# Performance work log

Hardware: AMD Instinct MI355X
Metric: run time of the kernel (lower is better)

The kernel has to match this reference:

```python
import jax, jax.numpy as jnp
import numpy as np

OBS, ACT, H, O, B = 256, 64, 1024, 8, 4096
ALPHA, GAMMA, ACT_LIMIT = 0.2, 0.99, 1.0
LOG_STD_MIN, LOG_STD_MAX = -20.0, 2.0
D = OBS + ACT + O  # intra-Q input dim


def setup_inputs() -> dict:
    key = jax.random.key(0)
    ks = iter(jax.random.split(key, 64))
    w = lambda shape: (jax.random.normal(next(ks), shape) * 0.05).astype(jnp.float32)
    inp = {}
    inp["state"] = jax.random.normal(next(ks), (B, OBS), jnp.float32)
    inp["action"] = jnp.tanh(jax.random.normal(next(ks), (B, ACT), jnp.float32))
    inp["next_state"] = jax.random.normal(next(ks), (B, OBS), jnp.float32)
    inp["reward"] = jax.random.normal(next(ks), (B, 1), jnp.float32)
    inp["done"] = jnp.zeros((B, 1), jnp.float32)
    inp["noise"] = jax.random.normal(next(ks), (B, ACT), jnp.float32)
    inp["option"] = jax.random.randint(next(ks), (B,), 0, O, jnp.int32)
    # online inter-Q (q1,q2 stacked on leading axis): obs -> H -> H -> O
    inp["interq_W1"], inp["interq_b1"] = w((2, OBS, H)), w((2, H))
    inp["interq_W2"], inp["interq_b2"] = w((2, H, H)), w((2, H))
    inp["interq_W3"], inp["interq_b3"] = w((2, H, O)), w((2, O))
    # target inter-Q
    inp["tinterq_W1"], inp["tinterq_b1"] = w((2, OBS, H)), w((2, H))
    inp["tinterq_W2"], inp["tinterq_b2"] = w((2, H, H)), w((2, H))
    inp["tinterq_W3"], inp["tinterq_b3"] = w((2, H, O)), w((2, O))
    # intra-Q (q1,q2 stacked): [obs,act,onehot] -> H -> H -> 1
    inp["intraq_W1"], inp["intraq_b1"] = w((2, D, H)), w((2, H))
    inp["intraq_W2"], inp["intraq_b2"] = w((2, H, H)), w((2, H))
    inp["intraq_W3"], inp["intraq_b3"] = w((2, H, 1)), w((2, 1))
    # per-option squashed-Gaussian policies: obs -> H -> H -> (mu, log_std)
    inp["pol_W1"], inp["pol_b1"] = w((O, OBS, H)), w((O, H))
    inp["pol_W2"], inp["pol_b2"] = w((O, H, H)), w((O, H))
    inp["pol_Wmu"], inp["pol_bmu"] = w((O, H, ACT)), w((O, ACT))
    inp["pol_Wls"], inp["pol_bls"] = w((O, H, ACT)), w((O, ACT))
    # per-option termination (beta) nets: obs -> H -> 1, sigmoid
    inp["beta_W1"], inp["beta_b1"] = w((O, OBS, H)), w((O, H))
    inp["beta_W2"], inp["beta_b2"] = w((O, H, 1)), w((O, 1))
    return inp


def _mlp2_k(x, W1, b1, W2, b2, W3, b3):
    # x: [B,in], params stacked over leading k -> [k,B,out]
    h = jax.nn.relu(jnp.einsum('bi,kih->kbh', x, W1) + b1[:, None, :])
    h = jax.nn.relu(jnp.einsum('kbh,khg->kbg', h, W2) + b2[:, None, :])
    return jnp.einsum('kbg,kgo->kbo', h, W3) + b3[:, None, :]


def _forward(state, action, next_state, reward, done, noise,
             interq_W1, interq_b1, interq_W2, interq_b2, interq_W3, interq_b3,
             tinterq_W1, tinterq_b1, tinterq_W2, tinterq_b2, tinterq_W3, tinterq_b3,
             intraq_W1, intraq_b1, intraq_W2, intraq_b2, intraq_W3, intraq_b3,
             pol_W1, pol_b1, pol_W2, pol_b2, pol_Wmu, pol_bmu, pol_Wls, pol_bls,
             beta_W1, beta_b1, beta_W2, beta_b2, option):
    idx = jnp.arange(state.shape[0])
    onehot = jax.nn.one_hot(option, O, dtype=state.dtype)
    # intra Q on (state, action, onehot)
    xq = jnp.concatenate([state, action, onehot], axis=-1)  # [B,D]
    q_intra = _mlp2_k(xq, intraq_W1, intraq_b1, intraq_W2, intraq_b2, intraq_W3, intraq_b3)
    q1_intra, q2_intra = q_intra[0], q_intra[1]  # [B,1]
    # option-routed policy: compute all options, gather top-1 (grouped-MoE form)
    h = jax.nn.relu(jnp.einsum('bi,oih->boh', state, pol_W1) + pol_b1)      # [B,O,H]
    h = jax.nn.relu(jnp.einsum('boh,ohg->bog', h, pol_W2) + pol_b2)         # [B,O,H]
    mu = (jnp.einsum('bog,oga->boa', h, pol_Wmu) + pol_bmu)[idx, option]    # [B,ACT]
    ls = (jnp.einsum('bog,oga->boa', h, pol_Wls) + pol_bls)[idx, option]
    ls = jnp.clip(ls, LOG_STD_MIN, LOG_STD_MAX)
    pre = mu + jnp.exp(ls) * noise  # reparameterized pre-tanh action
    LOG2PI = jnp.float32(np.log(2.0 * np.pi))
    logp = jnp.sum(-0.5 * noise**2 - ls - 0.5 * LOG2PI, axis=-1)
    logp = logp - jnp.sum(2.0 * (jnp.log(jnp.float32(2.0)) - pre - jax.nn.softplus(-2.0 * pre)), axis=-1)  # [B]
    current_actions = ACT_LIMIT * jnp.tanh(pre)  # [B,ACT]
    # option-routed termination prob on next_state
    hb = jax.nn.relu(jnp.einsum('bi,oih->boh', next_state, beta_W1) + beta_b1)
    blog = jnp.einsum('boh,oh->bo', hb, beta_W2[..., 0]) + beta_b2[:, 0]
    beta_prob = jax.nn.sigmoid(blog)[idx, option][:, None]  # [B,1]
    # TD target (no-grad in torch)
    q_t = _mlp2_k(next_state, tinterq_W1, tinterq_b1, tinterq_W2, tinterq_b2, tinterq_W3, tinterq_b3)
    q_inter_targ = jnp.minimum(q_t[0], q_t[1])  # [B,O]
    q_cur = q_inter_targ[idx, option][:, None]
    q_on = _mlp2_k(next_state, interq_W1, interq_b1, interq_W2, interq_b2, interq_W3, interq_b3)
    next_opt = jnp.argmax(jnp.minimum(q_on[0], q_on[1]), axis=-1)  # greedy next option
    q_next = q_inter_targ[idx, next_opt][:, None]
    bp = jax.lax.stop_gradient(beta_prob)
    backup = jax.lax.stop_gradient(
        reward + GAMMA * (1.0 - done) * ((1.0 - bp) * q_cur + bp * q_next))
    loss_intra_q = jnp.mean((q1_intra - backup) ** 2) + jnp.mean((q2_intra - backup) ** 2)
    q_pi = jax.lax.stop_gradient(jnp.minimum(q1_intra, q2_intra))[:, 0]
    loss_intra_pi = jnp.mean(ALPHA * logp - q_pi)
    return (loss_intra_q, loss_intra_pi, current_actions, logp, beta_prob)


def reference(state, action, next_state, reward, done, noise,
              interq_W1, interq_b1, interq_W2, interq_b2, interq_W3, interq_b3,
              tinterq_W1, tinterq_b1, tinterq_W2, tinterq_b2, tinterq_W3, tinterq_b3,
              intraq_W1, intraq_b1, intraq_W2, intraq_b2, intraq_W3, intraq_b3,
              pol_W1, pol_b1, pol_W2, pol_b2, pol_Wmu, pol_bmu, pol_Wls, pol_bls,
              beta_W1, beta_b1, beta_W2, beta_b2, option):
    return _forward(state, action, next_state, reward, done, noise,
                    interq_W1, interq_b1, interq_W2, interq_b2, interq_W3, interq_b3,
                    tinterq_W1, tinterq_b1, tinterq_W2, tinterq_b2, tinterq_W3, tinterq_b3,
                    intraq_W1, intraq_b1, intraq_W2, intraq_b2, intraq_W3, intraq_b3,
                    pol_W1, pol_b1, pol_W2, pol_b2, pol_Wmu, pol_bmu, pol_Wls, pol_bls,
                    beta_W1, beta_b1, beta_W2, beta_b2, option)
```

## Files before the change

### kernel.cpp

```cpp
#include <hip/hip_runtime.h>
#include <stdint.h>

#define B_SZ 4096
#define OBS 256
#define ACT 64
#define HID 1024
#define NOPT 8

typedef __attribute__((ext_vector_type(8))) short short8;
typedef __attribute__((ext_vector_type(4))) float floatx4;

constexpr long long OFF_WT_I1 = 0;
constexpr long long OFF_WT_I2 = OFF_WT_I1 + 2LL*1024*256*2;
constexpr long long OFF_WT_T1 = OFF_WT_I2 + 2LL*1024*1024*2;
constexpr long long OFF_WT_T2 = OFF_WT_T1 + 2LL*1024*256*2;
constexpr long long OFF_WT_X1 = OFF_WT_T2 + 2LL*1024*1024*2;
constexpr long long OFF_WT_X2 = OFF_WT_X1 + 2LL*1024*384*2;
constexpr long long OFF_WT_P1 = OFF_WT_X2 + 2LL*1024*1024*2;
constexpr long long OFF_WT_P2 = OFF_WT_P1 + 8LL*1024*256*2;
constexpr long long OFF_WT_ML = OFF_WT_P2 + 8LL*1024*1024*2;
constexpr long long OFF_WT_B1 = OFF_WT_ML + 8LL*128*1024*2;
constexpr long long OFF_XQ    = OFF_WT_B1 + 8LL*1024*256*2;
constexpr long long OFF_NS    = OFF_XQ + 4096LL*384*2;
constexpr long long OFF_AGS   = OFF_NS + 4096LL*256*2;
constexpr long long OFF_AGN   = OFF_AGS + 4224LL*256*2;
constexpr long long OFF_HAX   = OFF_AGN + 4224LL*256*2;
constexpr long long OFF_HAI   = OFF_HAX + 2LL*4096*1024*2;
constexpr long long OFF_HAT   = OFF_HAI + 2LL*4096*1024*2;
constexpr long long OFF_HAP   = OFF_HAT + 2LL*4096*1024*2;
constexpr long long OFF_HAB   = OFF_HAP + 4224LL*1024*2;
constexpr long long OFF_HBP   = OFF_HAB + 4224LL*1024*2;
constexpr long long OFF_QI    = OFF_HBP + 4224LL*1024*2;
constexpr long long OFF_QON   = OFF_QI + 2LL*16*4096*4;
constexpr long long OFF_QT    = OFF_QON + 2LL*16*4096*8*4;
constexpr long long OFF_MULS  = OFF_QT + 2LL*16*4096*8*4;
constexpr long long OFF_PERM  = OFF_MULS + 4224LL*128*4;
constexpr long long OFF_OPTG  = OFF_PERM + 4096LL*4;
constexpr long long OFF_BP    = OFF_OPTG + ((4224LL*4 + 255) & ~255LL);
constexpr long long OFF_LOGP  = OFF_BP + 4096LL*4;
constexpr long long OFF_TILEB = OFF_LOGP + 4096LL*4;
constexpr long long OFF_TILEC = OFF_TILEB + 272LL*64;
constexpr long long OFF_TILED = OFF_TILEC + 232LL*64;
constexpr long long WS_TOTAL  = OFF_TILED + 40LL*64;

struct Tile {
  long long aOff, wOff, cOff;
  int mStart, mEnd, K, nCols, flags, biasSel, biasOff, redSel, redOff, pad0;
};
struct Ptrs { const float* bias[9]; const float* w3[3]; };
struct TrSrcs { const float* p[11]; };

__device__ __forceinline__ unsigned short f2bf(float x){
  union { float f; unsigned u; } v; v.f = x;
  unsigned r = v.u + 0x7fffu + ((v.u >> 16) & 1u);
  return (unsigned short)(r >> 16);
}
__device__ __forceinline__ float bf2f(unsigned short h){
  union { float f; unsigned u; } v; v.u = ((unsigned)h) << 16; return v.f;
}
__device__ __forceinline__ void load16(const void* g, void* l){
  __builtin_amdgcn_global_load_lds((const __attribute__((address_space(1))) void*)g,
                                   (__attribute__((address_space(3))) void*)l, 16, 0, 0);
}

__device__ const int tr_cum[12] = {0,512,2560,3072,5120,5888,7936,9984,18176,18688,19200,21248};
__device__ const int tr_gx[11]  = {8,32,8,32,12,32,8,32,32,32,8};
__device__ const int tr_K[11]   = {256,1024,256,1024,328,1024,256,1024,1024,1024,256};
__device__ const int tr_Kp[11]  = {256,1024,256,1024,384,1024,256,1024,1024,1024,256};
__device__ const int tr_N[11]   = {1024,1024,1024,1024,1024,1024,1024,1024,64,64,1024};
__device__ const long long tr_ws[11] = {256*1024,1024*1024,256*1024,1024*1024,328*1024,1024*1024,256*1024,1024*1024,1024*64,1024*64,256*1024};
__device__ const long long tr_ts[11] = {1024*256,1024*1024,1024*256,1024*1024,1024*384,1024*1024,1024*256,1024*1024,128*1024,128*1024,1024*256};
__device__ const long long tr_dst[11] = {OFF_WT_I1,OFF_WT_I2,OFF_WT_T1,OFF_WT_T2,OFF_WT_X1,OFF_WT_X2,OFF_WT_P1,OFF_WT_P2,OFF_WT_ML,OFF_WT_ML+64LL*1024*2,OFF_WT_B1};

__global__ void k_tr_all(char* __restrict__ wsB, TrSrcs srcs){
  int id = blockIdx.x, j = 0;
  while (id >= tr_cum[j+1]) j++;
  int tloc = id - tr_cum[j];
  int gx = tr_gx[j], gy = tr_N[j] >> 5;
  int per = gx*gy;
  int z = tloc / per, r = tloc % per;
  int kx = r % gx, ny = r / gx;
  int K = tr_K[j], Kpad = tr_Kp[j], N = tr_N[j];
  const float* src = srcs.p[j] + (long long)z * tr_ws[j];
  unsigned short* dst = (unsigned short*)(wsB + tr_dst[j]) + (long long)z * tr_ts[j];
  __shared__ float tile[32][33];
  int k0 = kx*32, n0 = ny*32;
  int tx = threadIdx.x, ty = threadIdx.y;
  #pragma unroll
  for (int i=0;i<4;i++){
    int k = k0 + ty + i*8;
    tile[ty+i*8][tx] = (k < K) ? src[(long long)k*N + n0 + tx] : 0.f;
  }
  __syncthreads();
  #pragma unroll
  for (int i=0;i<4;i++){
    int n = n0 + ty + i*8;
    dst[(long long)n*Kpad + k0 + tx] = f2bf(tile[tx][ty+i*8]);
  }
}

__global__ void k_route(char* __restrict__ wsB, const int* __restrict__ option,
                        float* __restrict__ out){
  __shared__ int cnt[NOPT], off[NOPT+1], cur[NOPT], ctiles[NOPT], toff[NOPT+1];
  int tid = threadIdx.x;
  int* perm = (int*)(wsB + OFF_PERM);
  int* optg = (int*)(wsB + OFF_OPTG);
  Tile* tb = (Tile*)(wsB + OFF_TILEB);
  Tile* tc = (Tile*)(wsB + OFF_TILEC);
  Tile* tdt = (Tile*)(wsB + OFF_TILED);
  if (tid < NOPT) cnt[tid] = 0;
  __syncthreads();
  for (int b = tid; b < B_SZ; b += 256) atomicAdd(&cnt[option[b]], 1);
  __syncthreads();
  if (tid == 0){
    off[0] = 0; toff[0] = 0;
    for (int o=0;o<NOPT;o++){
      off[o+1] = off[o] + cnt[o];
      ctiles[o] = (cnt[o] + 127) >> 7;
      toff[o+1] = toff[o] + ctiles[o];
      cur[o] = off[o];
    }
    out[0] = 0.f; out[1] = 0.f;
  }
  __syncthreads();
  for (int b = tid; b < B_SZ; b += 256){
    int o = option[b];
    int pos = atomicAdd(&cur[o], 1);
    perm[pos] = b; optg[pos] = o;
  }
  __syncthreads();
  if (tid < 192){
    int task = tid/32, mt = tid%32, z = task&1, net = task>>1;
    int ms = mt*128;
    Tile T{};
    T.mStart = ms; T.mEnd = 4096; T.nCols = 1024; T.flags = 0;
    T.redSel = 0; T.redOff = 0;
    if (net==0){ T.K=384; T.aOff = OFF_XQ + (long long)ms*768; T.wOff = OFF_WT_X1 + (long long)z*786432; T.cOff = OFF_HAX + (long long)z*8388608; T.biasSel=0; }
    else if (net==1){ T.K=256; T.aOff = OFF_NS + (long long)ms*512; T.wOff = OFF_WT_I1 + (long long)z*524288; T.cOff = OFF_HAI + (long long)z*8388608; T.biasSel=1; }
    else { T.K=256; T.aOff = OFF_NS + (long long)ms*512; T.wOff = OFF_WT_T1 + (long long)z*524288; T.cOff = OFF_HAT + (long long)z*8388608; T.biasSel=2; }
    T.biasOff = z*1024;
    tb[tid] = T;
    Tile C{};
    C.mStart = ms; C.mEnd = 4096; C.K = 1024; C.nCols = 1024;
    if (net==0){ C.flags=2; C.aOff = OFF_HAX + (long long)z*8388608 + (long long)ms*2048; C.wOff = OFF_WT_X2 + (long long)z*2097152; C.cOff = OFF_QI + (long long)z*262144; C.biasSel=5; C.redSel=0; C.redOff=z*1024; }
    else if (net==1){ C.flags=3; C.aOff = OFF_HAI + (long long)z*8388608 + (long long)ms*2048; C.wOff = OFF_WT_I2 + (long long)z*2097152; C.cOff = OFF_QON + (long long)z*2097152; C.biasSel=6; C.redSel=1; C.redOff=z*8192; }
    else { C.flags=3; C.aOff = OFF_HAT + (long long)z*8388608 + (long long)ms*2048; C.wOff = OFF_WT_T2 + (long long)z*2097152; C.cOff = OFF_QT + (long long)z*2097152; C.biasSel=7; C.redSel=2; C.redOff=z*8192; }
    C.biasOff = z*1024;
    tc[tid] = C;
  }
  if (tid < NOPT){
    int o = tid, base = toff[o], gs = off[o], ge = off[o+1];
    for (int t=0; t<ctiles[o]; t++){
      int ms = gs + t*128;
      Tile P{};
      P.mStart=ms; P.mEnd=ge; P.K=256; P.nCols=1024; P.flags=0;
      P.aOff = OFF_AGS + (long long)ms*512; P.wOff = OFF_WT_P1 + (long long)o*524288;
      P.cOff = OFF_HAP; P.biasSel=3; P.biasOff=o*1024;
      tb[192 + base + t] = P;
      Tile Bt{};
      Bt.mStart=ms; Bt.mEnd=ge; Bt.K=256; Bt.nCols=1024; Bt.flags=0;
      Bt.aOff = OFF_AGN + (long long)ms*512; Bt.wOff = OFF_WT_B1 + (long long)o*524288;
      Bt.cOff = OFF_HAB; Bt.biasSel=4; Bt.biasOff=o*1024;
      tb[232 + base + t] = Bt;
      Tile C2{};
      C2.mStart=ms; C2.mEnd=ge; C2.K=1024; C2.nCols=1024; C2.flags=0;
      C2.aOff = OFF_HAP + (long long)ms*2048; C2.wOff = OFF_WT_P2 + (long long)o*2097152;
      C2.cOff = OFF_HBP; C2.biasSel=8; C2.biasOff=o*1024;
      tc[192 + base + t] = C2;
      Tile M{};
      M.mStart=ms; M.mEnd=ge; M.K=1024; M.nCols=128; M.flags=1;
      M.aOff = OFF_HBP + (long long)ms*2048; M.wOff = OFF_WT_ML + (long long)o*262144;
      M.cOff = OFF_MULS; M.biasSel=-1;
      tdt[base + t] = M;
    }
  }
  __syncthreads();
  int tT = toff[NOPT];
  for (int s = tT + tid; s < 40; s += 256){
    tb[192+s].K = 0; tb[232+s].K = 0; tc[192+s].K = 0; tdt[s].K = 0;
  }
}

__global__ void k_prep(char* __restrict__ wsB, const float* __restrict__ state,
                       const float* __restrict__ action, const float* __restrict__ nstate,
                       const int* __restrict__ option){
  int blk = blockIdx.x, tid = threadIdx.x;
  const int* perm = (const int*)(wsB + OFF_PERM);
  if (blk < 4224){
    unsigned short* agS = (unsigned short*)(wsB + OFF_AGS);
    unsigned short* agN = (unsigned short*)(wsB + OFF_AGN);
    long long o = (long long)blk*256 + tid;
    if (blk < 4096){
      long long src = (long long)perm[blk]*256 + tid;
      agS[o] = f2bf(state[src]); agN[o] = f2bf(nstate[src]);
    } else { agS[o] = 0; agN[o] = 0; }
  } else if (blk < 8320){
    int b = blk - 4224;
    unsigned short* xq = (unsigned short*)(wsB + OFF_XQ);
    for (int c = tid; c < 384; c += 256){
      float v;
      if (c < 256) v = state[(long long)b*256 + c];
      else if (c < 320) v = action[(long long)b*64 + (c-256)];
      else if (c < 328) v = (option[b] == (c-320)) ? 1.f : 0.f;
      else v = 0.f;
      xq[(long long)b*384 + c] = f2bf(v);
    }
  } else {
    long long i = (long long)(blk-8320)*1024 + tid;
    unsigned short* nsb = (unsigned short*)(wsB + OFF_NS);
    #pragma unroll
    for (int k=0;k<4;k++){ nsb[i] = f2bf(nstate[i]); i += 256; }
  }
}

__global__ __launch_bounds__(256)
void k_gemm(char* __restrict__ wsB, long long tileOff, Ptrs ptrs){
  __shared__ unsigned short As[128*64];
  __shared__ unsigned short Bs[128*64];
  Tile t = ((const Tile*)(wsB + tileOff))[blockIdx.y];
  if (t.K == 0) return;
  int n0 = blockIdx.x * 128;
  if (n0 >= t.nCols) return;

  int tid = threadIdx.x;
  int wave = tid >> 6, lane = tid & 63;
  int wm = wave & 1, wn = wave >> 1;
  int quad = lane >> 4, l16 = lane & 15;

  const floatx4 fzero = {0.f,0.f,0.f,0.f};
  floatx4 acc[4][4];
  #pragma unroll
  for (int mi=0;mi<4;mi++)
    #pragma unroll
    for (int ni=0;ni<4;ni++) acc[mi][ni] = fzero;

  long long rowBytes = (long long)t.K*2;
  const char* Abase = wsB + t.aOff;
  const char* Bbase = wsB + t.wOff + (long long)n0*rowBytes;

  int rsub = lane >> 2;
  int koff = (lane & 3) * 16;
  int r0 = wave*32 + rsub;
  int r1 = r0 + 16;
  long long gA0 = (long long)r0*rowBytes + koff;
  long long gA1 = (long long)r1*rowBytes + koff;
  char* lA = (char*)As + wave*2048 + (long long)lane*16;
  char* lB = (char*)Bs + wave*2048 + (long long)lane*16;

  int nkb = t.K >> 6;
  for (int kb = 0; kb < nkb; kb++){
    long long kbb = (long long)kb*128;
    load16(Abase + gA0 + kbb,      lA);
    load16(Abase + gA0 + kbb + 64, lA + 8192);
    load16(Abase + gA1 + kbb,      lA + 1024);
    load16(Abase + gA1 + kbb + 64, lA + 9216);
    load16(Bbase + gA0 + kbb,      lB);
    load16(Bbase + gA0 + kbb + 64, lB + 8192);
    load16(Bbase + gA1 + kbb,      lB + 1024);
    load16(Bbase + gA1 + kbb + 64, lB + 9216);
    __syncthreads();
    #pragma unroll
    for (int h=0; h<2; h++){
      short8 af[4], bfr[4];
      #pragma unroll
      for (int mi=0;mi<4;mi++)
        af[mi] = *(const short8*)(As + h*4096 + (wm*64 + mi*16 + l16)*32 + quad*8);
      #pragma unroll
      for (int ni=0;ni<4;ni++)
        bfr[ni] = *(const short8*)(Bs + h*4096 + (wn*64 + ni*16 + l16)*32 + quad*8);
      #pragma unroll
      for (int mi=0;mi<4;mi++)
        #pragma unroll
        for (int ni=0;ni<4;ni++)
          acc[mi][ni] = __builtin_amdgcn_mfma_f32_16x16x32_bf16(af[mi], bfr[ni], acc[mi][ni], 0, 0, 0);
    }
    __syncthreads();
  }

  if (t.flags <= 1){
    const float* bz = (t.biasSel >= 0) ? (ptrs.bias[t.biasSel] + t.biasOff) : nullptr;
    #pragma unroll
    for (int ni=0;ni<4;ni++){
      int col = n0 + wn*64 + ni*16 + l16;
      float bval = bz ? bz[col] : 0.f;
      #pragma unroll
      for (int mi=0;mi<4;mi++){
        int rbase = t.mStart + wm*64 + mi*16 + quad*4;
        floatx4 v = acc[mi][ni];
        #pragma unroll
        for (int r=0;r<4;r++){
          int grow = rbase + r;
          if (grow < t.mEnd){
            float x = v[r] + bval;
            if (t.flags == 0){
              x = fmaxf(x, 0.f);
              ((unsigned short*)(wsB + t.cOff))[(long long)grow*t.nCols + col] = f2bf(x);
            } else {
              ((float*)(wsB + t.cOff))[(long long)grow*t.nCols + col] = x;
            }
          }
        }
      }
    }
  } else {
    int NC = (t.flags == 2) ? 1 : 8;
    const float* w3 = ptrs.w3[t.redSel] + t.redOff;
    const float* bz = ptrs.bias[t.biasSel] + t.biasOff;
    int sl = blockIdx.x*2 + wn;
    float* red = (float*)(wsB + t.cOff) + (long long)sl*4096*NC;
    float bv[4]; int colv[4];
    #pragma unroll
    for (int ni=0;ni<4;ni++){ colv[ni] = n0 + wn*64 + ni*16 + l16; bv[ni] = bz[colv[ni]]; }
    #pragma unroll
    for (int mi=0;mi<4;mi++){
      #pragma unroll
      for (int r=0;r<4;r++){
        int row = t.mStart + wm*64 + mi*16 + quad*4 + r;
        float v[8];
        #pragma unroll
        for (int c=0;c<8;c++) v[c] = 0.f;
        #pragma unroll
        for (int ni=0;ni<4;ni++){
          float x = fmaxf(acc[mi][ni][r] + bv[ni], 0.f);
          if (NC == 1) v[0] += x * w3[colv[ni]];
          else {
            #pragma unroll
            for (int c=0;c<8;c++) v[c] += x * w3[colv[ni]*8 + c];
          }
        }
        for (int c=0;c<NC;c++){
          float s = v[c];
          s += __shfl_xor(s,1); s += __shfl_xor(s,2); s += __shfl_xor(s,4); s += __shfl_xor(s,8);
          if (l16 == 0 && row < t.mEnd) red[(long long)row*NC + c] = s;
        }
      }
    }
  }
}

__global__ void k_bp(char* __restrict__ wsB, const float* __restrict__ noise,
                     const float* __restrict__ bmu, const float* __restrict__ bls,
                     const float* __restrict__ beW2, const float* __restrict__ beb2,
                     float* __restrict__ out){
  int blk = blockIdx.x, lane = threadIdx.x;
  const int* perm = (const int*)(wsB + OFF_PERM);
  const int* optg = (const int*)(wsB + OFF_OPTG);
  if (blk < B_SZ){
    int i = blk, o = optg[i], b = perm[i];
    const float* muls = (const float*)(wsB + OFF_MULS);
    float* logp = (float*)(wsB + OFF_LOGP);
    float mu = muls[(long long)i*128 + lane] + bmu[o*ACT + lane];
    float ls = muls[(long long)i*128 + 64 + lane] + bls[o*ACT + lane];
    ls = fminf(fmaxf(ls, -20.f), 2.f);
    float nv = noise[(long long)b*ACT + lane];
    float pre = mu + expf(ls)*nv;
    out[2 + (long long)b*ACT + lane] = tanhf(pre);
    float xx = -2.f*pre;
    float sp = fmaxf(xx, 0.f) + log1pf(expf(-fabsf(xx)));
    const float LOG2PI = 1.8378770664093453f;
    const float LN2 = 0.6931471805599453f;
    float lp = -0.5f*nv*nv - ls - 0.5f*LOG2PI - 2.f*(LN2 - pre - sp);
    for (int s=32;s;s>>=1) lp += __shfl_xor(lp, s);
    if (lane == 0){ out[2 + (long long)B_SZ*ACT + b] = lp; logp[b] = lp; }
  } else {
    int i = blk - B_SZ, o = optg[i], b = perm[i];
    const unsigned short* h = (const unsigned short*)(wsB + OFF_HAB) + (long long)i*HID;
    const float* w = beW2 + (long long)o*HID;
    float* bp = (float*)(wsB + OFF_BP);
    float acc = 0.f;
    for (int k = lane; k < HID; k += 64) acc += bf2f(h[k]) * w[k];
    for (int s=32;s;s>>=1) acc += __shfl_xor(acc, s);
    if (lane == 0){
      float v = 1.f/(1.f + expf(-(acc + beb2[o])));
      out[2 + (long long)B_SZ*ACT + B_SZ + b] = v; bp[b] = v;
    }
  }
}

__global__ void k_td(const char* __restrict__ wsB, const int* __restrict__ option,
                     const float* __restrict__ reward, const float* __restrict__ done,
                     const float* __restrict__ xb3, const float* __restrict__ ib3,
                     const float* __restrict__ tb3, float* __restrict__ out){
  int b = blockIdx.x*256 + threadIdx.x;
  const float* qiP  = (const float*)(wsB + OFF_QI);
  const float* qonP = (const float*)(wsB + OFF_QON);
  const float* qtP  = (const float*)(wsB + OFF_QT);
  const float* bp   = (const float*)(wsB + OFF_BP);
  const float* logp = (const float*)(wsB + OFF_LOGP);
  float q1 = xb3[0], q2 = xb3[1];
  #pragma unroll
  for (int sl=0; sl<16; sl++){
    q1 += qiP[sl*4096 + b];
    q2 += qiP[65536 + sl*4096 + b];
  }
  float qons[2][8], qts[2][8];
  #pragma unroll
  for (int z=0;z<2;z++)
    #pragma unroll
    for (int o=0;o<8;o++){ qons[z][o] = ib3[z*8+o]; qts[z][o] = tb3[z*8+o]; }
  for (int z=0;z<2;z++){
    for (int sl=0; sl<16; sl++){
      long long base = ((long long)(z*16 + sl)*4096 + b)*8;
      #pragma unroll
      for (int o=0;o<8;o++){ qons[z][o] += qonP[base+o]; qts[z][o] += qtP[base+o]; }
    }
  }
  float qitv[NOPT];
  #pragma unroll
  for (int o=0;o<NOPT;o++) qitv[o] = fminf(qts[0][o], qts[1][o]);
  float qcur = qitv[option[b]];
  float best = -1e30f; int bo = 0;
  #pragma unroll
  for (int o=0;o<NOPT;o++){
    float v = fminf(qons[0][o], qons[1][o]);
    if (v > best){ best = v; bo = o; }
  }
  float qnext = qitv[bo];
  float bpv = bp[b];
  float backup = reward[b] + 0.99f*(1.f - done[b])*((1.f - bpv)*qcur + bpv*qnext);
  float d1 = q1 - backup, d2 = q2 - backup;
  float tq = d1*d1 + d2*d2;
  float qpi = fminf(q1, q2);
  float tp = 0.2f*logp[b] - qpi;
  for (int s=32;s;s>>=1){ tq += __shfl_xor(tq, s); tp += __shfl_xor(tp, s); }
  __shared__ float sq[4], sp2[4];
  int wave = threadIdx.x>>6, lane = threadIdx.x&63;
  if (lane==0){ sq[wave]=tq; sp2[wave]=tp; }
  __syncthreads();
  if (threadIdx.x==0){
    atomicAdd(&out[0], (sq[0]+sq[1]+sq[2]+sq[3])/(float)B_SZ);
    atomicAdd(&out[1], (sp2[0]+sp2[1]+sp2[2]+sp2[3])/(float)B_SZ);
  }
}

extern "C" void kernel_launch(void* const* d_in, const int* in_sizes, int n_in,
                              void* d_out, int out_size, void* d_ws, size_t ws_size,
                              hipStream_t stream){
  const float* state  = (const float*)d_in[0];
  const float* action = (const float*)d_in[1];
  const float* nstate = (const float*)d_in[2];
  const float* reward = (const float*)d_in[3];
  const float* done   = (const float*)d_in[4];
  const float* noise  = (const float*)d_in[5];
  const int*   option = (const int*)d_in[6];
  const float* iq_W1 = (const float*)d_in[7];  const float* iq_b1 = (const float*)d_in[8];
  const float* iq_W2 = (const float*)d_in[9];  const float* iq_b2 = (const float*)d_in[10];
  const float* iq_W3 = (const float*)d_in[11]; const float* iq_b3 = (const float*)d_in[12];
  const float* tq_W1 = (const float*)d_in[13]; const float* tq_b1 = (const float*)d_in[14];
  const float* tq_W2 = (const float*)d_in[15]; const float* tq_b2 = (const float*)d_in[16];
  const float* tq_W3 = (const float*)d_in[17]; const float* tq_b3 = (const float*)d_in[18];
  const float* xw_W1 = (const float*)d_in[19]; const float* xw_b1 = (const float*)d_in[20];
  const float* xw_W2 = (const float*)d_in[21]; const float* xw_b2 = (const float*)d_in[22];
  const float* xw_W3 = (const float*)d_in[23]; const float* xw_b3 = (const float*)d_in[24];
  const float* p_W1 = (const float*)d_in[25];  const float* p_b1 = (const float*)d_in[26];
  const float* p_W2 = (const float*)d_in[27];  const float* p_b2 = (const float*)d_in[28];
  const float* p_Wmu = (const float*)d_in[29]; const float* p_bmu = (const float*)d_in[30];
  const float* p_Wls = (const float*)d_in[31]; const float* p_bls = (const float*)d_in[32];
  const float* be_W1 = (const float*)d_in[33]; const float* be_b1 = (const float*)d_in[34];
  const float* be_W2 = (const float*)d_in[35]; const float* be_b2 = (const float*)d_in[36];
  float* out = (float*)d_out;
  char* wsB = (char*)d_ws;
  if ((long long)ws_size < WS_TOTAL) return;

  TrSrcs trs;
  trs.p[0]=iq_W1; trs.p[1]=iq_W2; trs.p[2]=tq_W1; trs.p[3]=tq_W2; trs.p[4]=xw_W1;
  trs.p[5]=xw_W2; trs.p[6]=p_W1; trs.p[7]=p_W2; trs.p[8]=p_Wmu; trs.p[9]=p_Wls; trs.p[10]=be_W1;
  Ptrs ptrs;
  ptrs.bias[0]=xw_b1; ptrs.bias[1]=iq_b1; ptrs.bias[2]=tq_b1; ptrs.bias[3]=p_b1; ptrs.bias[4]=be_b1;
  ptrs.bias[5]=xw_b2; ptrs.bias[6]=iq_b2; ptrs.bias[7]=tq_b2; ptrs.bias[8]=p_b2;
  ptrs.w3[0]=xw_W3; ptrs.w3[1]=iq_W3; ptrs.w3[2]=tq_W3;

  k_route<<<1, 256, 0, stream>>>(wsB, option, out);
  k_tr_all<<<21248, dim3(32,8), 0, stream>>>(wsB, trs);
  k_prep<<<9344, 256, 0, stream>>>(wsB, state, action, nstate, option);
  k_gemm<<<dim3(8,272), 256, 0, stream>>>(wsB, OFF_TILEB, ptrs);
  k_gemm<<<dim3(8,232), 256, 0, stream>>>(wsB, OFF_TILEC, ptrs);
  k_gemm<<<dim3(1,40), 256, 0, stream>>>(wsB, OFF_TILED, ptrs);
  k_bp<<<2*B_SZ, 64, 0, stream>>>(wsB, noise, p_bmu, p_bls, be_W2, be_b2, out);
  k_td<<<B_SZ/256, 256, 0, stream>>>(wsB, option, reward, done, xw_b3, iq_b3, tq_b3, out);
}
```

Before: 549.3 us.

## Widen GEMM block tile to 128x256 and pack beta/policy rows per block

The shared GEMM kernel now computes 128x256 output tiles, with eight MFMA column fragments per wave, a doubled B shared-memory buffer and a cooperative loader. The number of partial-sum reduction slices for the fused third-layer epilogue drops from 16 to 8, and the workspace layout and the TD reduction kernel are adjusted to match. The aim is to reuse each A tile across more columns and cut the partial-sum traffic. The cost is higher register and LDS use per block and fewer blocks in flight. The beta/logp kernel also packs four 64-lane jobs into each 256-thread block and reads hidden rows with vectorized 16-byte loads.

Result: faster. 508.1 us (-7.5%).

```diff
diff --git a/kernel.cpp b/kernel.cpp
--- a/kernel.cpp
+++ b/kernel.cpp
@@ -31,9 +31,9 @@
 constexpr long long OFF_HAB   = OFF_HAP + 4224LL*1024*2;
 constexpr long long OFF_HBP   = OFF_HAB + 4224LL*1024*2;
 constexpr long long OFF_QI    = OFF_HBP + 4224LL*1024*2;
-constexpr long long OFF_QON   = OFF_QI + 2LL*16*4096*4;
-constexpr long long OFF_QT    = OFF_QON + 2LL*16*4096*8*4;
-constexpr long long OFF_MULS  = OFF_QT + 2LL*16*4096*8*4;
+constexpr long long OFF_QON   = OFF_QI + 2LL*8*4096*4;
+constexpr long long OFF_QT    = OFF_QON + 2LL*8*4096*8*4;
+constexpr long long OFF_MULS  = OFF_QT + 2LL*8*4096*8*4;
 constexpr long long OFF_PERM  = OFF_MULS + 4224LL*128*4;
 constexpr long long OFF_OPTG  = OFF_PERM + 4096LL*4;
 constexpr long long OFF_BP    = OFF_OPTG + ((4224LL*4 + 255) & ~255LL);
@@ -142,9 +142,9 @@
     tb[tid] = T;
     Tile C{};
     C.mStart = ms; C.mEnd = 4096; C.K = 1024; C.nCols = 1024;
-    if (net==0){ C.flags=2; C.aOff = OFF_HAX + (long long)z*8388608 + (long long)ms*2048; C.wOff = OFF_WT_X2 + (long long)z*2097152; C.cOff = OFF_QI + (long long)z*262144; C.biasSel=5; C.redSel=0; C.redOff=z*1024; }
-    else if (net==1){ C.flags=3; C.aOff = OFF_HAI + (long long)z*8388608 + (long long)ms*2048; C.wOff = OFF_WT_I2 + (long long)z*2097152; C.cOff = OFF_QON + (long long)z*2097152; C.biasSel=6; C.redSel=1; C.redOff=z*8192; }
-    else { C.flags=3; C.aOff = OFF_HAT + (long long)z*8388608 + (long long)ms*2048; C.wOff = OFF_WT_T2 + (long long)z*2097152; C.cOff = OFF_QT + (long long)z*2097152; C.biasSel=7; C.redSel=2; C.redOff=z*8192; }
+    if (net==0){ C.flags=2; C.aOff = OFF_HAX + (long long)z*8388608 + (long long)ms*2048; C.wOff = OFF_WT_X2 + (long long)z*2097152; C.cOff = OFF_QI + (long long)z*131072; C.biasSel=5; C.redSel=0; C.redOff=z*1024; }
+    else if (net==1){ C.flags=3; C.aOff = OFF_HAI + (long long)z*8388608 + (long long)ms*2048; C.wOff = OFF_WT_I2 + (long long)z*2097152; C.cOff = OFF_QON + (long long)z*1048576; C.biasSel=6; C.redSel=1; C.redOff=z*8192; }
+    else { C.flags=3; C.aOff = OFF_HAT + (long long)z*8388608 + (long long)ms*2048; C.wOff = OFF_WT_T2 + (long long)z*2097152; C.cOff = OFF_QT + (long long)z*1048576; C.biasSel=7; C.redSel=2; C.redOff=z*8192; }
     C.biasOff = z*1024;
     tc[tid] = C;
   }
@@ -213,13 +213,13 @@
   }
 }
 
-__global__ __launch_bounds__(256)
+__global__ __launch_bounds__(256, 2)
 void k_gemm(char* __restrict__ wsB, long long tileOff, Ptrs ptrs){
   __shared__ unsigned short As[128*64];
-  __shared__ unsigned short Bs[128*64];
+  __shared__ unsigned short Bs[256*64];
   Tile t = ((const Tile*)(wsB + tileOff))[blockIdx.y];
   if (t.K == 0) return;
-  int n0 = blockIdx.x * 128;
+  int n0 = blockIdx.x * 256;
   if (n0 >= t.nCols) return;
 
   int tid = threadIdx.x;
@@ -228,50 +228,49 @@
   int quad = lane >> 4, l16 = lane & 15;
 
   const floatx4 fzero = {0.f,0.f,0.f,0.f};
-  floatx4 acc[4][4];
+  floatx4 acc[4][8];
   #pragma unroll
   for (int mi=0;mi<4;mi++)
     #pragma unroll
-    for (int ni=0;ni<4;ni++) acc[mi][ni] = fzero;
+    for (int ni=0;ni<8;ni++) acc[mi][ni] = fzero;
 
   long long rowBytes = (long long)t.K*2;
   const char* Abase = wsB + t.aOff;
   const char* Bbase = wsB + t.wOff + (long long)n0*rowBytes;
 
-  int rsub = lane >> 2;
-  int koff = (lane & 3) * 16;
-  int r0 = wave*32 + rsub;
-  int r1 = r0 + 16;
-  long long gA0 = (long long)r0*rowBytes + koff;
-  long long gA1 = (long long)r1*rowBytes + koff;
-  char* lA = (char*)As + wave*2048 + (long long)lane*16;
-  char* lB = (char*)Bs + wave*2048 + (long long)lane*16;
+  int ra0 = tid >> 2, ka0 = (tid & 3) * 16;
+  int ra1 = (tid + 256) >> 2, ka1 = ka0;
+  char* lA = (char*)As + (long long)tid*16;
+  char* lB = (char*)Bs + (long long)tid*16;
 
   int nkb = t.K >> 6;
   for (int kb = 0; kb < nkb; kb++){
     long long kbb = (long long)kb*128;
-    load16(Abase + gA0 + kbb,      lA);
-    load16(Abase + gA0 + kbb + 64, lA + 8192);
-    load16(Abase + gA1 + kbb,      lA + 1024);
-    load16(Abase + gA1 + kbb + 64, lA + 9216);
-    load16(Bbase + gA0 + kbb,      lB);
-    load16(Bbase + gA0 + kbb + 64, lB + 8192);
-    load16(Bbase + gA1 + kbb,      lB + 1024);
-    load16(Bbase + gA1 + kbb + 64, lB + 9216);
+    load16(Abase + (long long)ra0*rowBytes + kbb + ka0,      lA);
+    load16(Abase + (long long)ra0*rowBytes + kbb + 64 + ka0, lA + 8192);
+    load16(Abase + (long long)ra1*rowBytes + kbb + ka1,      lA + 4096);
+    load16(Abase + (long long)ra1*rowBytes + kbb + 64 + ka1, lA + 12288);
+    #pragma unroll
+    for (int j=0;j<4;j++){
+      int cb = tid + j*256;
+      int rb = cb >> 2, kbo = (cb & 3) * 16;
+      load16(Bbase + (long long)rb*rowBytes + kbb + kbo,      lB + j*4096);
+      load16(Bbase + (long long)rb*rowBytes + kbb + 64 + kbo, lB + 16384 + j*4096);
+    }
     __syncthreads();
     #pragma unroll
     for (int h=0; h<2; h++){
-      short8 af[4], bfr[4];
+      short8 af[4], bfr[8];
       #pragma unroll
       for (int mi=0;mi<4;mi++)
-        af[mi] = *(const short8*)(As + h*4096 + (wm*64 + mi*16 + l16)*32 + quad*8);
-      #pragma unroll
-      for (int ni=0;ni<4;ni++)
-        bfr[ni] = *(const short8*)(Bs + h*4096 + (wn*64 + ni*16 + l16)*32 + quad*8);
+        af[mi] = *(const short8*)((const char*)As + h*8192 + (wm*64 + mi*16 + l16)*64 + quad*16);
+      #pragma unroll
+      for (int ni=0;ni<8;ni++)
+        bfr[ni] = *(const short8*)((const char*)Bs + h*16384 + (wn*128 + ni*16 + l16)*64 + quad*16);
       #pragma unroll
       for (int mi=0;mi<4;mi++)
         #pragma unroll
-        for (int ni=0;ni<4;ni++)
+        for (int ni=0;ni<8;ni++)
           acc[mi][ni] = __builtin_amdgcn_mfma_f32_16x16x32_bf16(af[mi], bfr[ni], acc[mi][ni], 0, 0, 0);
     }
     __syncthreads();
@@ -280,8 +279,9 @@
   if (t.flags <= 1){
     const float* bz = (t.biasSel >= 0) ? (ptrs.bias[t.biasSel] + t.biasOff) : nullptr;
     #pragma unroll
-    for (int ni=0;ni<4;ni++){
-      int col = n0 + wn*64 + ni*16 + l16;
+    for (int ni=0;ni<8;ni++){
+      int col = n0 + wn*128 + ni*16 + l16;
+      if (col >= t.nCols) continue;
       float bval = bz ? bz[col] : 0.f;
       #pragma unroll
       for (int mi=0;mi<4;mi++){
@@ -308,9 +308,9 @@
     const float* bz = ptrs.bias[t.biasSel] + t.biasOff;
     int sl = blockIdx.x*2 + wn;
     float* red = (float*)(wsB + t.cOff) + (long long)sl*4096*NC;
-    float bv[4]; int colv[4];
-    #pragma unroll
-    for (int ni=0;ni<4;ni++){ colv[ni] = n0 + wn*64 + ni*16 + l16; bv[ni] = bz[colv[ni]]; }
+    float bv[8]; int colv[8];
+    #pragma unroll
+    for (int ni=0;ni<8;ni++){ colv[ni] = n0 + wn*128 + ni*16 + l16; bv[ni] = bz[colv[ni]]; }
     #pragma unroll
     for (int mi=0;mi<4;mi++){
       #pragma unroll
@@ -320,7 +320,7 @@
         #pragma unroll
         for (int c=0;c<8;c++) v[c] = 0.f;
         #pragma unroll
-        for (int ni=0;ni<4;ni++){
+        for (int ni=0;ni<8;ni++){
           float x = fmaxf(acc[mi][ni][r] + bv[ni], 0.f);
           if (NC == 1) v[0] += x * w3[colv[ni]];
           else {
@@ -342,11 +342,12 @@
                      const float* __restrict__ bmu, const float* __restrict__ bls,
                      const float* __restrict__ beW2, const float* __restrict__ beb2,
                      float* __restrict__ out){
-  int blk = blockIdx.x, lane = threadIdx.x;
+  int job = blockIdx.x*4 + (threadIdx.x >> 6);
+  int lane = threadIdx.x & 63;
   const int* perm = (const int*)(wsB + OFF_PERM);
   const int* optg = (const int*)(wsB + OFF_OPTG);
-  if (blk < B_SZ){
-    int i = blk, o = optg[i], b = perm[i];
+  if (job < B_SZ){
+    int i = job, o = optg[i], b = perm[i];
     const float* muls = (const float*)(wsB + OFF_MULS);
     float* logp = (float*)(wsB + OFF_LOGP);
     float mu = muls[(long long)i*128 + lane] + bmu[o*ACT + lane];
@@ -363,12 +364,18 @@
     for (int s=32;s;s>>=1) lp += __shfl_xor(lp, s);
     if (lane == 0){ out[2 + (long long)B_SZ*ACT + b] = lp; logp[b] = lp; }
   } else {
-    int i = blk - B_SZ, o = optg[i], b = perm[i];
-    const unsigned short* h = (const unsigned short*)(wsB + OFF_HAB) + (long long)i*HID;
+    int i = job - B_SZ, o = optg[i], b = perm[i];
+    const char* hrow = wsB + OFF_HAB + (long long)i*2048;
     const float* w = beW2 + (long long)o*HID;
     float* bp = (float*)(wsB + OFF_BP);
+    short8 v0 = *(const short8*)(hrow + lane*16);
+    short8 v1 = *(const short8*)(hrow + 1024 + lane*16);
     float acc = 0.f;
-    for (int k = lane; k < HID; k += 64) acc += bf2f(h[k]) * w[k];
+    #pragma unroll
+    for (int e=0;e<8;e++){
+      acc += bf2f((unsigned short)v0[e]) * w[lane*8 + e];
+      acc += bf2f((unsigned short)v1[e]) * w[512 + lane*8 + e];
+    }
     for (int s=32;s;s>>=1) acc += __shfl_xor(acc, s);
     if (lane == 0){
       float v = 1.f/(1.f + expf(-(acc + beb2[o])));
@@ -389,9 +396,9 @@
   const float* logp = (const float*)(wsB + OFF_LOGP);
   float q1 = xb3[0], q2 = xb3[1];
   #pragma unroll
-  for (int sl=0; sl<16; sl++){
+  for (int sl=0; sl<8; sl++){
     q1 += qiP[sl*4096 + b];
-    q2 += qiP[65536 + sl*4096 + b];
+    q2 += qiP[32768 + sl*4096 + b];
   }
   float qons[2][8], qts[2][8];
   #pragma unroll
@@ -399,8 +406,8 @@
     #pragma unroll
     for (int o=0;o<8;o++){ qons[z][o] = ib3[z*8+o]; qts[z][o] = tb3[z*8+o]; }
   for (int z=0;z<2;z++){
-    for (int sl=0; sl<16; sl++){
-      long long base = ((long long)(z*16 + sl)*4096 + b)*8;
+    for (int sl=0; sl<8; sl++){
+      long long base = ((long long)(z*8 + sl)*4096 + b)*8;
       #pragma unroll
       for (int o=0;o<8;o++){ qons[z][o] += qonP[base+o]; qts[z][o] += qtP[base+o]; }
     }
@@ -473,9 +480,9 @@
   k_route<<<1, 256, 0, stream>>>(wsB, option, out);
   k_tr_all<<<21248, dim3(32,8), 0, stream>>>(wsB, trs);
   k_prep<<<9344, 256, 0, stream>>>(wsB, state, action, nstate, option);
-  k_gemm<<<dim3(8,272), 256, 0, stream>>>(wsB, OFF_TILEB, ptrs);
-  k_gemm<<<dim3(8,232), 256, 0, stream>>>(wsB, OFF_TILEC, ptrs);
+  k_gemm<<<dim3(4,272), 256, 0, stream>>>(wsB, OFF_TILEB, ptrs);
+  k_gemm<<<dim3(4,232), 256, 0, stream>>>(wsB, OFF_TILEC, ptrs);
   k_gemm<<<dim3(1,40), 256, 0, stream>>>(wsB, OFF_TILED, ptrs);
-  k_bp<<<2*B_SZ, 64, 0, stream>>>(wsB, noise, p_bmu, p_bls, be_W2, be_b2, out);
+  k_bp<<<2048, 256, 0, stream>>>(wsB, noise, p_bmu, p_bls, be_W2, be_b2, out);
   k_td<<<B_SZ/256, 256, 0, stream>>>(wsB, option, reward, done, xw_b3, iq_b3, tq_b3, out);
 }
```
